# Optimization experiments

Measured on AMD Instinct MI355X. Metric: run time of the kernel, lower is better.

## Reference

```python
import jax, jax.numpy as jnp
import numpy as np

N_NODES = 100000
N_EDGES = 3200000

def setup_inputs() -> dict:
    key = jax.random.key(0)
    ks = jax.random.split(key, 6)
    x = jax.random.normal(ks[0], (N_NODES, 40), dtype=jnp.float32)
    src = jax.random.randint(ks[1], (N_EDGES,), 0, N_NODES, dtype=jnp.int32)
    dst = jax.random.randint(ks[2], (N_EDGES,), 0, N_NODES, dtype=jnp.int32)
    W1 = jax.random.normal(ks[3], (10, 128), dtype=jnp.float32) * 0.1
    b1 = jnp.zeros((128,), dtype=jnp.float32)
    W2 = jax.random.normal(ks[4], (128, 64), dtype=jnp.float32) * 0.1
    b2 = jnp.zeros((64,), dtype=jnp.float32)
    return {"x": x, "src": src, "dst": dst, "W1": W1, "b1": b1, "W2": W2, "b2": b2}


def reference(x, src, dst, W1, b1, W2, b2):
    N = x.shape[0]
    xs = x[:, 15:25]  # forward slices features to in_dim=10
    ones = jnp.ones(src.shape[0], dtype=x.dtype)
    deg_out = jax.ops.segment_sum(ones, src, num_segments=N)  # out-degree of src nodes
    deg_in = jax.ops.segment_sum(ones, dst, num_segments=N)   # in-degree of dst nodes
    # DGL GraphConv norm='both': clamp zero degrees to 1, symmetric 1/sqrt norm
    norm_s = jnp.where(deg_out > 0, deg_out, 1.0) ** -0.5
    norm_d = jnp.where(deg_in > 0, deg_in, 1.0) ** -0.5
    # aggregate-then-transform (in_dim < hidden_dim path in DGL)
    msgs = (xs * norm_s[:, None])[src]                         # [E, 10]
    agg = jax.ops.segment_sum(msgs, dst, num_segments=N)      # [N, 10]
    agg = agg * norm_d[:, None]
    h = agg @ W1 + b1                                          # GraphConv weight + bias
    return h @ W2 + b2                                         # linear head
```

## Files before the change

### kernel.cpp

```cpp
#include <hip/hip_runtime.h>
#include <hip/hip_fp16.h>


#define NF    10
#define COLS  40
#define OFF   15
#define H1    128
#define H2    64

#define BSH   7
#define BW    128
#define NBIN  782
#define NBINP 784
#define GS    16
#define RND   16u
#define CAPH  6400
#define PRCAP 4864
#define SENT  0xFFFFFFFFu
#define NBLKB 320
#define CHUNK 10000

#define DBLK    128
#define DCHUNKS 32
#define DRANGES 4
#define DRNG    25000
#define DRNG4   6250
#define DEDGE   100000

typedef unsigned int u32;
typedef unsigned short u16;
typedef unsigned char u8;

__device__ __forceinline__ float2 h2f(u32 u) {
    __half2 h;
    *reinterpret_cast<u32*>(&h) = u;
    return __half22float2(h);
}
__device__ __forceinline__ u32 f2h(float a, float b) {
    __half2 h = __float22half2_rn(make_float2(a, b));
    return *reinterpret_cast<u32*>(&h);
}

__global__ void __launch_bounds__(256, 2)
fusedA_kernel(const int* __restrict__ src, const int* __restrict__ dst,
              const float* __restrict__ W1, const float* __restrict__ b1,
              const float* __restrict__ W2, const float* __restrict__ b2,
              float* __restrict__ Wc, float* __restrict__ bc,
              u32* __restrict__ gcur, u32* __restrict__ partial32,
              u32* __restrict__ srt, int E, int N) {
    __shared__ union {
        struct { u32 hist[NBINP], lofs[NBINP], gbase[NBINP], lcur[NBINP];
                 u32 stage[CHUNK]; u16 sbin[CHUNK]; } pb;
        struct { u32 cnt[DRNG4]; } dg;
    } sh;
    int blk = blockIdx.x;
    int t = threadIdx.x;

    if (blk < DBLK) {
        int c = blk & (DCHUNKS - 1);
        int r = blk >> 5;
        u32* cnt = sh.dg.cnt;
        for (int i = t; i < DRNG4; i += 256) cnt[i] = 0;
        __syncthreads();
        int base = r * DRNG;
        int e0 = c * DEDGE, e1 = min(E, e0 + DEDGE);
        int nv4 = (e1 - e0) >> 2;
        const int4* s4 = (const int4*)(src + e0);
        for (int i = t; i < nv4; i += 256) {
            int4 s = s4[i];
            int a0 = s.x - base, a1 = s.y - base, a2 = s.z - base, a3 = s.w - base;
            if ((u32)a0 < (u32)DRNG) atomicAdd(&cnt[a0 >> 2], 1u << ((a0 & 3) << 3));
            if ((u32)a1 < (u32)DRNG) atomicAdd(&cnt[a1 >> 2], 1u << ((a1 & 3) << 3));
            if ((u32)a2 < (u32)DRNG) atomicAdd(&cnt[a2 >> 2], 1u << ((a2 & 3) << 3));
            if ((u32)a3 < (u32)DRNG) atomicAdd(&cnt[a3 >> 2], 1u << ((a3 & 3) << 3));
        }
        __syncthreads();
        u32* d32 = partial32 + ((size_t)c * N + base) / 4;
        for (int i = t; i < DRNG4; i += 256) d32[i] = cnt[i];
    } else if (blk < DBLK + NBLKB) {
        u32* hist = sh.pb.hist;
        u32* lofs = sh.pb.lofs;
        u32* gbase = sh.pb.gbase;
        u32* lcur = sh.pb.lcur;
        u32* stage = sh.pb.stage;
        u16* sbin = sh.pb.sbin;
        for (int i = t; i < NBINP; i += 256) hist[i] = 0;
        __syncthreads();

        int e0 = (blk - DBLK) * CHUNK;
        int m = min(E - e0, CHUNK);
        int m4 = m >> 2;
        const int4* d4 = (const int4*)(dst + e0);
        const int4* s4 = (const int4*)(src + e0);

        for (int i4 = t; i4 < m4; i4 += 256) {
            int4 d = d4[i4];
            atomicAdd(&hist[d.x >> BSH], 1u);
            atomicAdd(&hist[d.y >> BSH], 1u);
            atomicAdd(&hist[d.z >> BSH], 1u);
            atomicAdd(&hist[d.w >> BSH], 1u);
        }
        for (int e = e0 + 4 * m4 + t; e < e0 + m; e += 256)
            atomicAdd(&hist[dst[e] >> BSH], 1u);
        __syncthreads();

        if (t < 64) {
            u32 c[13];
            u32 seg = 0;
#pragma unroll
            for (int q = 0; q < 13; ++q) {
                int idx = t * 13 + q;
                c[q] = (idx < NBINP) ? hist[idx] : 0u;
                seg += c[q];
            }
            u32 x = seg;
#pragma unroll
            for (int off = 1; off < 64; off <<= 1) {
                u32 v = (u32)__shfl_up((int)x, off, 64);
                if (t >= off) x += v;
            }
            u32 run = x - seg;
#pragma unroll
            for (int q = 0; q < 13; ++q) {
                int idx = t * 13 + q;
                if (idx < NBINP) lofs[idx] = run;
                run += c[q];
            }
        }
        __syncthreads();

        for (int b = t; b < NBIN; b += 256) {
            u32 h = hist[b];
            u32 r = (h + (RND - 1u)) & ~(RND - 1u);
            gbase[b] = r ? atomicAdd(&gcur[b * GS], r) : 0u;
            lcur[b] = lofs[b];
        }
        __syncthreads();

        for (int i4 = t; i4 < m4; i4 += 256) {
            int4 d = d4[i4];
            int4 s = s4[i4];
#define SC1(d_, s_) { int b_ = (d_) >> BSH; u32 p_ = atomicAdd(&lcur[b_], 1u); \
        stage[p_] = ((u32)(s_) << BSH) | (u32)((d_) & (BW - 1)); sbin[p_] = (u16)b_; }
            SC1(d.x, s.x); SC1(d.y, s.y); SC1(d.z, s.z); SC1(d.w, s.w);
        }
        for (int e = e0 + 4 * m4 + t; e < e0 + m; e += 256) {
            int d_ = dst[e], s_ = src[e];
            SC1(d_, s_);
        }
#undef SC1
        __syncthreads();

        for (int i = t; i < m; i += 256) {
            u32 b = sbin[i];
            u32 idx = gbase[b] + (u32)i - lofs[b];
            if (idx < CAPH) srt[(size_t)b * CAPH + idx] = stage[i];
        }
        for (int b = t; b < NBIN; b += 256) {
            u32 h = hist[b];
            if (!h) continue;
            u32 r = (h + (RND - 1u)) & ~(RND - 1u);
            for (u32 k = h; k < r; ++k) {
                u32 idx = gbase[b] + k;
                if (idx < CAPH) srt[(size_t)b * CAPH + idx] = SENT;
            }
        }
    } else {
        for (int i = t; i < NF * H2; i += 256) {
            int k = i >> 6, j = i & 63;
            float acc = 0.f;
            for (int mm = 0; mm < H1; ++mm) acc += W1[k * H1 + mm] * W2[mm * H2 + j];
            Wc[i] = acc;
        }
        for (int j = t; j < H2; j += 256) {
            float a = b2[j];
            for (int mm = 0; mm < H1; ++mm) a += b1[mm] * W2[mm * H2 + j];
            bc[j] = a;
        }
    }
}

__global__ void __launch_bounds__(256)
xsn_kernel(const float* __restrict__ x, const u8* __restrict__ partial,
           u16* __restrict__ xsn, int N) {
    int n = blockIdx.x * blockDim.x + threadIdx.x;
    if (n >= N) return;
    u32 d = 0;
#pragma unroll 4
    for (int c = 0; c < DCHUNKS; ++c) d += partial[(size_t)c * N + n];
    float norm = rsqrtf(d > 0 ? (float)d : 1.f);
    const float* xr = x + (size_t)n * COLS + OFF;
    float v[NF];
#pragma unroll
    for (int k = 0; k < NF; ++k) v[k] = xr[k] * norm;
    uint4* xo = (uint4*)(xsn + ((size_t)n << 4));
    uint4 w0, w1;
    w0.x = f2h(v[0], v[1]); w0.y = f2h(v[2], v[3]);
    w0.z = f2h(v[4], v[5]); w0.w = f2h(v[6], v[7]);
    w1.x = f2h(v[8], v[9]); w1.y = 0u; w1.z = 0u; w1.w = 0u;
    xo[0] = w0;
    xo[1] = w1;
}

__global__ void __launch_bounds__(256, 6)
passC_kernel(const u32* __restrict__ srt, const u32* __restrict__ gcur,
             const u16* __restrict__ xsn, const float* __restrict__ Wc,
             const float* __restrict__ bc, float* __restrict__ out, int N) {
    __shared__ u32 sorted[PRCAP];
    __shared__ u32 cnt[BW];
    __shared__ u32 cur[BW];
    __shared__ float sW[NF * H2];
    __shared__ float sb[H2];
    int t = threadIdx.x;
    for (int i = t; i < NF * H2; i += 256) sW[i] = Wc[i];
    if (t < H2) sb[t] = bc[t];
    if (t < BW) cnt[t] = 0;
    __syncthreads();

    int b = blockIdx.x;
    const u32* reg = srt + (size_t)b * CAPH;
    u32 m = gcur[b * GS];
    if (m > CAPH) m = CAPH;

    for (u32 e = t; e < m; e += 256) {
        u32 v = reg[e];
        if (v != SENT) atomicAdd(&cnt[v & (BW - 1)], 1u);
    }
    __syncthreads();

    if (t < 64) {
        u32 c0 = cnt[t * 2], c1 = cnt[t * 2 + 1];
        u32 seg = c0 + c1;
        u32 x = seg;
#pragma unroll
        for (int off = 1; off < 64; off <<= 1) {
            u32 v = (u32)__shfl_up((int)x, off, 64);
            if (t >= off) x += v;
        }
        u32 run = x - seg;
        cur[t * 2] = run; run += c0;
        cur[t * 2 + 1] = run;
    }
    __syncthreads();

    for (u32 e = t; e < m; e += 256) {
        u32 v = reg[e];
        if (v == SENT) continue;
        u32 p = atomicAdd(&cur[v & (BW - 1)], 1u);
        if (p < PRCAP) sorted[p] = v >> BSH;
    }
    __syncthreads();

    int node_local = t >> 2;
    int j = t & 3;
    int jb = j << 4;
#pragma unroll
    for (int sub = 0; sub < 2; ++sub) {
        int node = sub * 64 + node_local;
        u32 c   = cnt[node];
        u32 end = cur[node];
        if (end > PRCAP) end = PRCAP;
        u32 st  = (end >= c) ? end - c : 0u;
        float r0=0.f,r1=0.f,r2=0.f,r3=0.f,r4=0.f,r5=0.f,r6=0.f,r7=0.f,r8=0.f,r9=0.f;
#pragma unroll 2
        for (u32 e = st + j; e < end; e += 4) {
            const u32* xr = (const u32*)(xsn + ((size_t)sorted[e] << 4));
            uint4 p0 = *(const uint4*)xr;
            u32 p1 = xr[4];
            float2 f;
            f = h2f(p0.x); r0 += f.x; r1 += f.y;
            f = h2f(p0.y); r2 += f.x; r3 += f.y;
            f = h2f(p0.z); r4 += f.x; r5 += f.y;
            f = h2f(p0.w); r6 += f.x; r7 += f.y;
            f = h2f(p1);   r8 += f.x; r9 += f.y;
        }
#define QRED(r) r += __shfl_xor(r, 1, 64); r += __shfl_xor(r, 2, 64)
        QRED(r0); QRED(r1); QRED(r2); QRED(r3); QRED(r4);
        QRED(r5); QRED(r6); QRED(r7); QRED(r8); QRED(r9);
#undef QRED
        int n = (b << BSH) + node;
        if (n < N) {
            float norm = rsqrtf(c > 0 ? (float)c : 1.f);
            r0 *= norm; r1 *= norm; r2 *= norm; r3 *= norm; r4 *= norm;
            r5 *= norm; r6 *= norm; r7 *= norm; r8 *= norm; r9 *= norm;
            float o[16];
#pragma unroll
            for (int q = 0; q < 16; ++q) o[q] = sb[jb + q];
            float rr[NF] = {r0,r1,r2,r3,r4,r5,r6,r7,r8,r9};
#pragma unroll
            for (int k = 0; k < NF; ++k) {
                float a = rr[k];
#pragma unroll
                for (int q = 0; q < 16; ++q) o[q] += a * sW[k * H2 + jb + q];
            }
            float* op = out + (size_t)n * H2 + jb;
            *(float4*)(op)      = make_float4(o[0], o[1], o[2], o[3]);
            *(float4*)(op + 4)  = make_float4(o[4], o[5], o[6], o[7]);
            *(float4*)(op + 8)  = make_float4(o[8], o[9], o[10], o[11]);
            *(float4*)(op + 12) = make_float4(o[12], o[13], o[14], o[15]);
        }
    }
}

extern "C" void kernel_launch(void* const* d_in, const int* in_sizes, int n_in,
                              void* d_out, int out_size, void* d_ws, size_t ws_size,
                              hipStream_t stream) {
    const float* x   = (const float*)d_in[0];
    const int*   src = (const int*)d_in[1];
    const int*   dst = (const int*)d_in[2];
    const float* W1  = (const float*)d_in[3];
    const float* b1  = (const float*)d_in[4];
    const float* W2  = (const float*)d_in[5];
    const float* b2  = (const float*)d_in[6];
    float* out = (float*)d_out;

    const int N = in_sizes[0] / COLS;
    const int E = in_sizes[1];

    float* ws = (float*)d_ws;
    float* Wc   = ws;
    float* bc   = Wc + NF * H2;
    u32*   gcur = (u32*)(bc + H2);
    size_t off_u32 = (size_t)(NF * H2 + H2) + (size_t)NBIN * GS;
    off_u32 = (off_u32 + 15) & ~(size_t)15;
    u16*   xsn = (u16*)((u32*)d_ws + off_u32);
    u32*   srt = (u32*)d_ws + off_u32 + (size_t)N * 8;
    u32*   partial32 = srt + (size_t)NBIN * CAPH;
    const u8* partial8 = (const u8*)partial32;

    hipMemsetAsync(gcur, 0, (size_t)NBIN * GS * sizeof(u32), stream);

    fusedA_kernel<<<DBLK + NBLKB + 1, 256, 0, stream>>>(
        src, dst, W1, b1, W2, b2, Wc, bc, gcur, partial32, srt, E, N);

    xsn_kernel<<<(N + 255) / 256, 256, 0, stream>>>(x, partial8, xsn, N);

    passC_kernel<<<NBIN, 256, 0, stream>>>(srt, gcur, xsn, Wc, bc, out, N);
}
```

Before: 193.6 us.

## Double fusedA block size and shrink staged bin ids to bytes

Launches the fused degree/binning kernel with 512 threads per block instead of 256 and updates all strided loops to match. Stores per-edge bin ids as u8 instead of u16 in shared memory, recovering the high bits from prefix-offset thresholds at bins 256, 512 and 768. This shrinks the LDS footprint and adds more threads per block to hide atomic and memory latency, at the cost of a few extra compares per scattered edge. The scan step still uses only 64 threads, and the launch-bound occupancy hint changes from 2 to 4.

```diff
diff --git a/kernel.cpp b/kernel.cpp
--- a/kernel.cpp
+++ b/kernel.cpp
@@ -19,6 +19,7 @@
 #define SENT  0xFFFFFFFFu
 #define NBLKB 320
 #define CHUNK 10000
+#define BT    512
 
 #define DBLK    128
 #define DCHUNKS 32
@@ -41,7 +42,7 @@
     return *reinterpret_cast<u32*>(&h);
 }
 
-__global__ void __launch_bounds__(256, 2)
+__global__ void __launch_bounds__(BT, 4)
 fusedA_kernel(const int* __restrict__ src, const int* __restrict__ dst,
               const float* __restrict__ W1, const float* __restrict__ b1,
               const float* __restrict__ W2, const float* __restrict__ b2,
@@ -50,7 +51,7 @@
               u32* __restrict__ srt, int E, int N) {
     __shared__ union {
         struct { u32 hist[NBINP], lofs[NBINP], gbase[NBINP], lcur[NBINP];
-                 u32 stage[CHUNK]; u16 sbin[CHUNK]; } pb;
+                 u32 stage[CHUNK]; u8 sbin[CHUNK]; } pb;
         struct { u32 cnt[DRNG4]; } dg;
     } sh;
     int blk = blockIdx.x;
@@ -60,13 +61,13 @@
         int c = blk & (DCHUNKS - 1);
         int r = blk >> 5;
         u32* cnt = sh.dg.cnt;
-        for (int i = t; i < DRNG4; i += 256) cnt[i] = 0;
+        for (int i = t; i < DRNG4; i += BT) cnt[i] = 0;
         __syncthreads();
         int base = r * DRNG;
         int e0 = c * DEDGE, e1 = min(E, e0 + DEDGE);
         int nv4 = (e1 - e0) >> 2;
         const int4* s4 = (const int4*)(src + e0);
-        for (int i = t; i < nv4; i += 256) {
+        for (int i = t; i < nv4; i += BT) {
             int4 s = s4[i];
             int a0 = s.x - base, a1 = s.y - base, a2 = s.z - base, a3 = s.w - base;
             if ((u32)a0 < (u32)DRNG) atomicAdd(&cnt[a0 >> 2], 1u << ((a0 & 3) << 3));
@@ -76,15 +77,15 @@
         }
         __syncthreads();
         u32* d32 = partial32 + ((size_t)c * N + base) / 4;
-        for (int i = t; i < DRNG4; i += 256) d32[i] = cnt[i];
+        for (int i = t; i < DRNG4; i += BT) d32[i] = cnt[i];
     } else if (blk < DBLK + NBLKB) {
         u32* hist = sh.pb.hist;
         u32* lofs = sh.pb.lofs;
         u32* gbase = sh.pb.gbase;
         u32* lcur = sh.pb.lcur;
         u32* stage = sh.pb.stage;
-        u16* sbin = sh.pb.sbin;
-        for (int i = t; i < NBINP; i += 256) hist[i] = 0;
+        u8*  sbin = sh.pb.sbin;
+        for (int i = t; i < NBINP; i += BT) hist[i] = 0;
         __syncthreads();
 
         int e0 = (blk - DBLK) * CHUNK;
@@ -93,14 +94,14 @@
         const int4* d4 = (const int4*)(dst + e0);
         const int4* s4 = (const int4*)(src + e0);
 
-        for (int i4 = t; i4 < m4; i4 += 256) {
+        for (int i4 = t; i4 < m4; i4 += BT) {
             int4 d = d4[i4];
             atomicAdd(&hist[d.x >> BSH], 1u);
             atomicAdd(&hist[d.y >> BSH], 1u);
             atomicAdd(&hist[d.z >> BSH], 1u);
             atomicAdd(&hist[d.w >> BSH], 1u);
         }
-        for (int e = e0 + 4 * m4 + t; e < e0 + m; e += 256)
+        for (int e = e0 + 4 * m4 + t; e < e0 + m; e += BT)
             atomicAdd(&hist[dst[e] >> BSH], 1u);
         __syncthreads();
 
@@ -129,7 +130,7 @@
         }
         __syncthreads();
 
-        for (int b = t; b < NBIN; b += 256) {
+        for (int b = t; b < NBIN; b += BT) {
             u32 h = hist[b];
             u32 r = (h + (RND - 1u)) & ~(RND - 1u);
             gbase[b] = r ? atomicAdd(&gcur[b * GS], r) : 0u;
@@ -137,26 +138,31 @@
         }
         __syncthreads();
 
-        for (int i4 = t; i4 < m4; i4 += 256) {
+        for (int i4 = t; i4 < m4; i4 += BT) {
             int4 d = d4[i4];
             int4 s = s4[i4];
 #define SC1(d_, s_) { int b_ = (d_) >> BSH; u32 p_ = atomicAdd(&lcur[b_], 1u); \
-        stage[p_] = ((u32)(s_) << BSH) | (u32)((d_) & (BW - 1)); sbin[p_] = (u16)b_; }
+        stage[p_] = ((u32)(s_) << BSH) | (u32)((d_) & (BW - 1)); sbin[p_] = (u8)b_; }
             SC1(d.x, s.x); SC1(d.y, s.y); SC1(d.z, s.z); SC1(d.w, s.w);
         }
-        for (int e = e0 + 4 * m4 + t; e < e0 + m; e += 256) {
+        for (int e = e0 + 4 * m4 + t; e < e0 + m; e += BT) {
             int d_ = dst[e], s_ = src[e];
             SC1(d_, s_);
         }
 #undef SC1
         __syncthreads();
 
-        for (int i = t; i < m; i += 256) {
-            u32 b = sbin[i];
-            u32 idx = gbase[b] + (u32)i - lofs[b];
-            if (idx < CAPH) srt[(size_t)b * CAPH + idx] = stage[i];
-        }
-        for (int b = t; b < NBIN; b += 256) {
+        {
+            u32 th1 = lofs[256], th2 = lofs[512], th3 = lofs[768];
+            for (int i = t; i < m; i += BT) {
+                u32 ui = (u32)i;
+                u32 k = (u32)(ui >= th1) + (u32)(ui >= th2) + (u32)(ui >= th3);
+                u32 b = (k << 8) + sbin[i];
+                u32 idx = gbase[b] + ui - lofs[b];
+                if (idx < CAPH) srt[(size_t)b * CAPH + idx] = stage[i];
+            }
+        }
+        for (int b = t; b < NBIN; b += BT) {
             u32 h = hist[b];
             if (!h) continue;
             u32 r = (h + (RND - 1u)) & ~(RND - 1u);
@@ -166,13 +172,13 @@
             }
         }
     } else {
-        for (int i = t; i < NF * H2; i += 256) {
+        for (int i = t; i < NF * H2; i += BT) {
             int k = i >> 6, j = i & 63;
             float acc = 0.f;
             for (int mm = 0; mm < H1; ++mm) acc += W1[k * H1 + mm] * W2[mm * H2 + j];
             Wc[i] = acc;
         }
-        for (int j = t; j < H2; j += 256) {
+        for (int j = t; j < H2; j += BT) {
             float a = b2[j];
             for (int mm = 0; mm < H1; ++mm) a += b1[mm] * W2[mm * H2 + j];
             bc[j] = a;
@@ -330,7 +336,7 @@
 
     hipMemsetAsync(gcur, 0, (size_t)NBIN * GS * sizeof(u32), stream);
 
-    fusedA_kernel<<<DBLK + NBLKB + 1, 256, 0, stream>>>(
+    fusedA_kernel<<<DBLK + NBLKB + 1, BT, 0, stream>>>(
         src, dst, W1, b1, W2, b2, Wc, bc, gcur, partial32, srt, E, N);
 
     xsn_kernel<<<(N + 255) / 256, 256, 0, stream>>>(x, partial8, xsn, N);
```

Result: faster. 179.5 us (-7.3%).
